# Kernel optimization log

Hardware: AMD Instinct MI355X
Metric: run time of the kernel (lower is better)

The kernel has to match this reference:

```python
import jax, jax.numpy as jnp
import numpy as np

IN_CH, OUT_CH, H, E, DOUT, MODES = 512, 512, 8, 64, 64, 64
B, LQ, LKV = 32, 1024, 1024


def setup_inputs() -> dict:
    key = jax.random.key(0)
    kq, kk, kv, kwr, kwi = jax.random.split(key, 5)
    scale = 1.0 / (IN_CH * OUT_CH)
    return {
        "q": jax.random.normal(kq, (B, LQ, H, E), jnp.float32),
        "k": jax.random.normal(kk, (B, LKV, H, E), jnp.float32),
        "v": jax.random.normal(kv, (B, LKV, H, E), jnp.float32),
        "mask": jnp.zeros((B, LQ), jnp.bool_),
        # complex parameter stored as (real, imag) pair; torch init is scale*rand -> U[0, scale)
        "weights_real": scale * jax.random.uniform(kwr, (H, E, DOUT, MODES), jnp.float32),
        "weights_imag": scale * jax.random.uniform(kwi, (H, E, DOUT, MODES), jnp.float32),
        # 'lowest' mode selection: arange(modes); all modes valid since LQ//2+1 > 63
        "index_q": jnp.arange(MODES, dtype=jnp.int32),
        "index_kv": jnp.arange(MODES, dtype=jnp.int32),
    }


def reference(q, k, v, mask, weights_real, weights_imag, index_q, index_kv):
    Lq = q.shape[1]
    # (B, L, H, E) -> (B, H, E, L)
    xq = jnp.transpose(q, (0, 2, 3, 1))
    xk = jnp.transpose(k, (0, 2, 3, 1))
    xq_ft = jnp.fft.rfft(xq.astype(jnp.float32), axis=-1)   # (B,H,E,Lq//2+1) c64
    xk_ft = jnp.fft.rfft(xk.astype(jnp.float32), axis=-1)
    xq_sel = xq_ft[..., index_q]    # (B,H,E,Mq) mode gather
    xk_sel = xk_ft[..., index_kv]   # (B,H,E,Mkv)
    # complex attention scores: xq_sel.mT @ xk_sel (no conjugation, matching torch)
    xqk = jnp.einsum("bhex,bhey->bhxy", xq_sel, xk_sel)     # (B,H,Mq,Mkv)
    # 'tanh' activation applied to real and imag parts separately
    xqk = jax.lax.complex(jnp.tanh(xqk.real), jnp.tanh(xqk.imag))
    w = jax.lax.complex(weights_real, weights_imag)         # (H,E,DOUT,Mq)
    xqkvw = jnp.einsum("bhxy,bhey,heox->bhox", xqk, xk_sel, w)  # (B,H,DOUT,Mq)
    # scatter selected modes back into zero spectrum, then inverse FFT
    freq_len_q = Lq // 2 + 1
    out_ft = jnp.zeros(xqkvw.shape[:3] + (freq_len_q,), jnp.complex64)
    out_ft = out_ft.at[..., index_q].set(xqkvw)
    out = jnp.fft.irfft(out_ft / (IN_CH * OUT_CH), n=Lq, axis=-1)  # (B,H,DOUT,Lq)
    return out.astype(q.dtype)
```

## Files before the change

kernel.cpp:

```cpp
#include <hip/hip_runtime.h>
#include <math.h>

#define OFF_WTR   262144u
#define OFF_WTI   2359296u
#define OFF_XQR   4456448u
#define OFF_XQI   5505024u
#define OFF_XKR   6553600u
#define OFF_XKI   7602176u
#define OFF_UR    8650752u
#define OFF_UI    9699328u
#define OFF_YR    10747904u
#define OFF_YI    11796480u

#define PI_F 3.14159265358979323846f

typedef __attribute__((ext_vector_type(8))) short bf16x8;
typedef __attribute__((ext_vector_type(4))) float f32x4;

__device__ inline unsigned short f2bf(float f) {
    unsigned u = __float_as_uint(f);
    unsigned r = u + 0x7FFFu + ((u >> 16) & 1u);
    return (unsigned short)(r >> 16);
}
__device__ inline float bf2f(unsigned short h) {
    return __uint_as_float(((unsigned)h) << 16);
}
__device__ inline void make_hilo8(const float* s, bf16x8& h, bf16x8& l) {
#pragma unroll
    for (int j = 0; j < 8; ++j) {
        unsigned short hb = f2bf(s[j]);
        h[j] = (short)hb;
        l[j] = (short)f2bf(s[j] - bf2f(hb));
    }
}
__device__ inline float twval(int m, int t, bool neg_sin) {
    int r = (m * t) & 1023;
    float ang = (float)r * (2.0f * PI_F / 1024.0f);
    float s, c;
    sincosf(ang, &s, &c);
    return neg_sin ? -s : c;
}

__global__ void k_tables(unsigned short* __restrict__ tab) {
    int idx = blockIdx.x * 256 + threadIdx.x;
    {
        int j = idx & 7, lane = (idx >> 3) & 63, nt = (idx >> 9) & 7, kt = idx >> 12;
        int k = kt * 32 + ((lane >> 4) << 3) + j;
        int n = nt * 16 + (lane & 15);
        float v = twval(n & 63, k, n >= 64);
        unsigned short hb = f2bf(v);
        tab[idx] = hb;
        tab[131072 + idx] = f2bf(v - bf2f(hb));
    }
    {
        int j = idx & 7, lane = (idx >> 3) & 63, ks = (idx >> 9) & 3, nt = idx >> 11;
        int kap = ks * 32 + ((lane >> 4) << 3) + j;
        int t = nt * 16 + (lane & 15);
        float v = twval(kap & 63, t, kap >= 64);
        unsigned short hb = f2bf(v);
        tab[262144 + idx] = hb;
        tab[393216 + idx] = f2bf(v - bf2f(hb));
    }
}

__global__ __launch_bounds__(256) void k_wt(const float* __restrict__ wr,
                                            const float* __restrict__ wi,
                                            float* __restrict__ ws) {
    __shared__ float tile[64 * 65];
    int he = blockIdx.x;
    int h = he >> 6, e = he & 63;
    const float* srcs[2] = { wr + (size_t)he * 4096, wi + (size_t)he * 4096 };
    float* dsts[2] = { ws + OFF_WTR, ws + OFF_WTI };
    for (int p = 0; p < 2; ++p) {
        __syncthreads();
        {
            int x = threadIdx.x & 63, orow = threadIdx.x >> 6;
            for (int i = 0; i < 16; ++i) {
                int o = orow * 16 + i;
                tile[o * 65 + x] = srcs[p][o * 64 + x];
            }
        }
        __syncthreads();
        {
            int o = threadIdx.x & 63, xrow = threadIdx.x >> 6;
            for (int i = 0; i < 16; ++i) {
                int x = xrow * 16 + i;
                dsts[p][(((size_t)h * 64 + x) * 64 + e) * 64 + o] = tile[o * 65 + x];
            }
        }
    }
}

__global__ __launch_bounds__(256, 2) void k_dft(const float* __restrict__ q,
                                                const float* __restrict__ kk,
                                                float* __restrict__ ws) {
    int blk = blockIdx.x;
    int src = blk >> 8;
    int bh = blk & 255;
    int b = bh >> 3, h = bh & 7;
    const float* A = src ? kk : q;
    const unsigned short* BDH = (const unsigned short*)ws;
    const unsigned short* BDL = BDH + 131072;

    __shared__ float Ald[64 * 68];

    int tid = threadIdx.x;
    int lane = tid & 63, wv = tid >> 6;
    int mhalf = wv & 1, nhalf = wv >> 1;

    f32x4 acc[2][4];
#pragma unroll
    for (int a = 0; a < 2; ++a)
#pragma unroll
        for (int c = 0; c < 4; ++c) acc[a][c] = (f32x4){0.f, 0.f, 0.f, 0.f};

    for (int kc = 0; kc < 16; ++kc) {
        __syncthreads();
        int t0 = kc * 64;
        int e0 = (tid & 15) * 4;
#pragma unroll
        for (int it = 0; it < 4; ++it) {
            int tl = it * 16 + (tid >> 4);
            float4 a = *(const float4*)(A + (((size_t)b * 1024 + t0 + tl) * 8 + h) * 64 + e0);
            Ald[(e0 + 0) * 68 + tl] = a.x;
            Ald[(e0 + 1) * 68 + tl] = a.y;
            Ald[(e0 + 2) * 68 + tl] = a.z;
            Ald[(e0 + 3) * 68 + tl] = a.w;
        }
        __syncthreads();
#pragma unroll
        for (int k2 = 0; k2 < 2; ++k2) {
            int ktile = kc * 2 + k2;
            bf16x8 ah[2], al[2];
#pragma unroll
            for (int mt = 0; mt < 2; ++mt) {
                int e = mhalf * 32 + mt * 16 + (lane & 15);
                int tt = k2 * 32 + (lane >> 4) * 8;
                float4 p0 = *(const float4*)&Ald[e * 68 + tt];
                float4 p1 = *(const float4*)&Ald[e * 68 + tt + 4];
                float f[8] = { p0.x, p0.y, p0.z, p0.w, p1.x, p1.y, p1.z, p1.w };
                make_hilo8(f, ah[mt], al[mt]);
            }
#pragma unroll
            for (int ntl = 0; ntl < 4; ++ntl) {
                int nt = nhalf * 4 + ntl;
                size_t off = (((size_t)ktile * 8 + nt) * 64 + lane) * 8;
                bf16x8 bh = *(const bf16x8*)(BDH + off);
                bf16x8 bl = *(const bf16x8*)(BDL + off);
#pragma unroll
                for (int mt = 0; mt < 2; ++mt) {
                    acc[mt][ntl] = __builtin_amdgcn_mfma_f32_16x16x32_bf16(ah[mt], bh, acc[mt][ntl], 0, 0, 0);
                    acc[mt][ntl] = __builtin_amdgcn_mfma_f32_16x16x32_bf16(ah[mt], bl, acc[mt][ntl], 0, 0, 0);
                    acc[mt][ntl] = __builtin_amdgcn_mfma_f32_16x16x32_bf16(al[mt], bh, acc[mt][ntl], 0, 0, 0);
                }
            }
        }
    }

    float* outR = ws + (src ? OFF_XKR : OFF_XQR) + (size_t)bh * 4096;
    float* outI = ws + (src ? OFF_XKI : OFF_XQI) + (size_t)bh * 4096;
#pragma unroll
    for (int mt = 0; mt < 2; ++mt)
#pragma unroll
        for (int ntl = 0; ntl < 4; ++ntl) {
            int n = (nhalf * 4 + ntl) * 16 + (lane & 15);
            float* dst = (n < 64) ? (outR + (n & 63)) : (outI + (n & 63));
            int erow0 = mhalf * 32 + mt * 16 + (lane >> 4) * 4;
#pragma unroll
            for (int r = 0; r < 4; ++r)
                dst[(erow0 + r) * 64] = acc[mt][ntl][r];
        }
}

__global__ __launch_bounds__(256, 1) void k_attn(float* __restrict__ ws) {
    __shared__ float bufA[8192];
    __shared__ float bufB[8192];
    int bh = blockIdx.x;
    int tid = threadIdx.x;
    const float* XqR = ws + OFF_XQR + (size_t)bh * 4096;
    const float* XqI = ws + OFF_XQI + (size_t)bh * 4096;
    const float* XkR = ws + OFF_XKR + (size_t)bh * 4096;
    const float* XkI = ws + OFF_XKI + (size_t)bh * 4096;
    for (int i = tid; i < 4096; i += 256) {
        bufA[i] = XqR[i]; bufA[4096 + i] = XqI[i];
        bufB[i] = XkR[i]; bufB[4096 + i] = XkI[i];
    }
    __syncthreads();

    int x4 = tid & 15, y4 = tid >> 4;
    int x0 = x4 * 4, y0 = y4 * 4;
    float Sr[4][4], Si[4][4];
#pragma unroll
    for (int a = 0; a < 4; ++a)
#pragma unroll
        for (int bidx = 0; bidx < 4; ++bidx) { Sr[a][bidx] = 0.f; Si[a][bidx] = 0.f; }
#pragma unroll 8
    for (int e = 0; e < 64; ++e) {
        float4 qr = *(const float4*)&bufA[e * 64 + x0];
        float4 qi = *(const float4*)&bufA[4096 + e * 64 + x0];
        float4 kr = *(const float4*)&bufB[e * 64 + y0];
        float4 ki = *(const float4*)&bufB[4096 + e * 64 + y0];
        float qra[4] = { qr.x, qr.y, qr.z, qr.w };
        float qia[4] = { qi.x, qi.y, qi.z, qi.w };
        float kra[4] = { kr.x, kr.y, kr.z, kr.w };
        float kia[4] = { ki.x, ki.y, ki.z, ki.w };
#pragma unroll
        for (int xi = 0; xi < 4; ++xi)
#pragma unroll
            for (int yi = 0; yi < 4; ++yi) {
                Sr[xi][yi] += qra[xi] * kra[yi] - qia[xi] * kia[yi];
                Si[xi][yi] += qra[xi] * kia[yi] + qia[xi] * kra[yi];
            }
    }
#pragma unroll
    for (int xi = 0; xi < 4; ++xi)
#pragma unroll
        for (int yi = 0; yi < 4; ++yi) {
            Sr[xi][yi] = tanhf(Sr[xi][yi]);
            Si[xi][yi] = tanhf(Si[xi][yi]);
        }
    __syncthreads();

#pragma unroll
    for (int xi = 0; xi < 4; ++xi)
#pragma unroll
        for (int yi = 0; yi < 4; ++yi) {
            bufA[(y0 + yi) * 64 + x0 + xi] = Sr[xi][yi];
            bufA[4096 + (y0 + yi) * 64 + x0 + xi] = Si[xi][yi];
        }
    float tR[16], tI[16];
#pragma unroll
    for (int j = 0; j < 16; ++j) {
        int idx = tid + 256 * j;
        tR[j] = bufB[idx]; tI[j] = bufB[4096 + idx];
    }
    __syncthreads();
#pragma unroll
    for (int j = 0; j < 16; ++j) {
        int idx = tid + 256 * j;
        int e = idx >> 6, m = idx & 63;
        bufB[m * 64 + e] = tR[j];
        bufB[4096 + m * 64 + e] = tI[j];
    }
    __syncthreads();

    int e4 = tid & 15, xb4 = tid >> 4;
    int e0 = e4 * 4, xb0 = xb4 * 4;
    float uR[4][4], uI[4][4];
#pragma unroll
    for (int a = 0; a < 4; ++a)
#pragma unroll
        for (int bidx = 0; bidx < 4; ++bidx) { uR[a][bidx] = 0.f; uI[a][bidx] = 0.f; }
#pragma unroll 8
    for (int y = 0; y < 64; ++y) {
        float4 sr = *(const float4*)&bufA[y * 64 + xb0];
        float4 si = *(const float4*)&bufA[4096 + y * 64 + xb0];
        float4 kr = *(const float4*)&bufB[y * 64 + e0];
        float4 ki = *(const float4*)&bufB[4096 + y * 64 + e0];
        float sra[4] = { sr.x, sr.y, sr.z, sr.w };
        float sia[4] = { si.x, si.y, si.z, si.w };
        float kra[4] = { kr.x, kr.y, kr.z, kr.w };
        float kia[4] = { ki.x, ki.y, ki.z, ki.w };
#pragma unroll
        for (int ei = 0; ei < 4; ++ei)
#pragma unroll
            for (int xi = 0; xi < 4; ++xi) {
                uR[ei][xi] += sra[xi] * kra[ei] - sia[xi] * kia[ei];
                uI[ei][xi] += sra[xi] * kia[ei] + sia[xi] * kra[ei];
            }
    }
    int b = bh >> 3, h = bh & 7;
    float* uRp = ws + OFF_UR;
    float* uIp = ws + OFF_UI;
#pragma unroll
    for (int xi = 0; xi < 4; ++xi) {
        size_t base = (((size_t)h * 64 + (xb0 + xi)) * 32 + b) * 64 + e0;
        float4 vr = { uR[0][xi], uR[1][xi], uR[2][xi], uR[3][xi] };
        float4 vi = { uI[0][xi], uI[1][xi], uI[2][xi], uI[3][xi] };
        *(float4*)&uRp[base] = vr;
        *(float4*)&uIp[base] = vi;
    }
}

__global__ __launch_bounds__(256, 2) void k_uw(float* __restrict__ ws) {
    __shared__ float su[2 * 2176];
    __shared__ float sw[2 * 4096];
    int hx = blockIdx.x;
    int tid = threadIdx.x;
    const float* uRp = ws + OFF_UR + (size_t)hx * 2048;
    const float* uIp = ws + OFF_UI + (size_t)hx * 2048;
    const float* wRp = ws + OFF_WTR + (size_t)hx * 4096;
    const float* wIp = ws + OFF_WTI + (size_t)hx * 4096;
    for (int i = tid; i < 2048; i += 256) {
        int b = i >> 6, e = i & 63;
        su[b * 68 + e] = uRp[i];
        su[2176 + b * 68 + e] = uIp[i];
    }
    for (int i = tid; i < 4096; i += 256) {
        sw[i] = wRp[i];
        sw[4096 + i] = wIp[i];
    }
    __syncthreads();
    int o16 = tid & 15, b8 = tid >> 4;
    int o0 = o16 * 4, b0 = b8 * 2;
    float aR[2][4], aI[2][4];
#pragma unroll
    for (int bi = 0; bi < 2; ++bi)
#pragma unroll
        for (int oi = 0; oi < 4; ++oi) { aR[bi][oi] = 0.f; aI[bi][oi] = 0.f; }
#pragma unroll 8
    for (int e = 0; e < 64; ++e) {
        float u0r = su[(b0 + 0) * 68 + e], u0i = su[2176 + (b0 + 0) * 68 + e];
        float u1r = su[(b0 + 1) * 68 + e], u1i = su[2176 + (b0 + 1) * 68 + e];
        float4 wr = *(const float4*)&sw[e * 64 + o0];
        float4 wi = *(const float4*)&sw[4096 + e * 64 + o0];
        float wra[4] = { wr.x, wr.y, wr.z, wr.w };
        float wia[4] = { wi.x, wi.y, wi.z, wi.w };
#pragma unroll
        for (int oi = 0; oi < 4; ++oi) {
            aR[0][oi] += u0r * wra[oi] - u0i * wia[oi];
            aI[0][oi] += u0r * wia[oi] + u0i * wra[oi];
            aR[1][oi] += u1r * wra[oi] - u1i * wia[oi];
            aI[1][oi] += u1r * wia[oi] + u1i * wra[oi];
        }
    }
    float* YRp = ws + OFF_YR + (size_t)hx * 2048;
    float* YIp = ws + OFF_YI + (size_t)hx * 2048;
#pragma unroll
    for (int bi = 0; bi < 2; ++bi) {
        float4 vr = { aR[bi][0], aR[bi][1], aR[bi][2], aR[bi][3] };
        float4 vi = { aI[bi][0], aI[bi][1], aI[bi][2], aI[bi][3] };
        *(float4*)&YRp[(b0 + bi) * 64 + o0] = vr;
        *(float4*)&YIp[(b0 + bi) * 64 + o0] = vi;
    }
}

__global__ __launch_bounds__(512, 2) void k_idft(const float* __restrict__ ws,
                                                 float* __restrict__ out) {
    __shared__ float Acoef[64 * 132];
    int bh = blockIdx.x;
    int b = bh >> 3, h = bh & 7;
    int tid = threadIdx.x;
    int lane = tid & 63, wv = tid >> 6;
    const float S0 = 3.7252902984619140625e-09f;
    const float* YRp = ws + OFF_YR;
    const float* YIp = ws + OFF_YI;
    const unsigned short* BIH = (const unsigned short*)ws + 262144;
    const unsigned short* BIL = (const unsigned short*)ws + 393216;

    for (int i = tid; i < 4096; i += 512) {
        int m = i >> 6, o = i & 63;
        size_t src = ((size_t)h * 64 + m) * 2048 + (size_t)b * 64 + o;
        float sca = (m == 0 ? 1.f : 2.f) * S0;
        Acoef[o * 132 + m] = YRp[src] * sca;
        Acoef[o * 132 + 64 + m] = YIp[src] * sca;
    }
    __syncthreads();

    bf16x8 ah[4][4], al[4][4];
#pragma unroll
    for (int mt = 0; mt < 4; ++mt)
#pragma unroll
        for (int ks = 0; ks < 4; ++ks) {
            int o = mt * 16 + (lane & 15);
            int kap0 = ks * 32 + (lane >> 4) * 8;
            float4 p0 = *(const float4*)&Acoef[o * 132 + kap0];
            float4 p1 = *(const float4*)&Acoef[o * 132 + kap0 + 4];
            float f[8] = { p0.x, p0.y, p0.z, p0.w, p1.x, p1.y, p1.z, p1.w };
            make_hilo8(f, ah[mt][ks], al[mt][ks]);
        }

    float* outp = out + ((size_t)b * 8 + h) * 65536;
#pragma unroll 2
    for (int ntl = 0; ntl < 8; ++ntl) {
        int nt = wv * 8 + ntl;
        f32x4 acc[4];
#pragma unroll
        for (int mt = 0; mt < 4; ++mt) acc[mt] = (f32x4){0.f, 0.f, 0.f, 0.f};
#pragma unroll
        for (int ks = 0; ks < 4; ++ks) {
            size_t off = (((size_t)nt * 4 + ks) * 64 + lane) * 8;
            bf16x8 bh = *(const bf16x8*)(BIH + off);
            bf16x8 bl = *(const bf16x8*)(BIL + off);
#pragma unroll
            for (int mt = 0; mt < 4; ++mt) {
                acc[mt] = __builtin_amdgcn_mfma_f32_16x16x32_bf16(ah[mt][ks], bh, acc[mt], 0, 0, 0);
                acc[mt] = __builtin_amdgcn_mfma_f32_16x16x32_bf16(ah[mt][ks], bl, acc[mt], 0, 0, 0);
                acc[mt] = __builtin_amdgcn_mfma_f32_16x16x32_bf16(al[mt][ks], bh, acc[mt], 0, 0, 0);
            }
        }
        int t = nt * 16 + (lane & 15);
#pragma unroll
        for (int mt = 0; mt < 4; ++mt) {
            int o0 = mt * 16 + (lane >> 4) * 4;
#pragma unroll
            for (int r = 0; r < 4; ++r)
                outp[(size_t)(o0 + r) * 1024 + t] = acc[mt][r];
        }
    }
}

extern "C" void kernel_launch(void* const* d_in, const int* in_sizes, int n_in,
                              void* d_out, int out_size, void* d_ws, size_t ws_size,
                              hipStream_t stream) {
    const float* q = (const float*)d_in[0];
    const float* k = (const float*)d_in[1];
    const float* wr = (const float*)d_in[4];
    const float* wi = (const float*)d_in[5];
    float* out = (float*)d_out;
    float* ws = (float*)d_ws;

    k_tables<<<512, 256, 0, stream>>>((unsigned short*)d_ws);
    k_wt<<<512, 256, 0, stream>>>(wr, wi, ws);
    k_dft<<<512, 256, 0, stream>>>(q, k, ws);
    k_attn<<<256, 256, 0, stream>>>(ws);
    k_uw<<<512, 256, 0, stream>>>(ws);
    k_idft<<<256, 512, 0, stream>>>(ws, out);
}
```

Measured before the change: 341.1 us.

## Move attention and weight contractions to split-bf16 MFMA and split DFT/IDFT work

The scalar FP32 complex matmuls in k_attn and k_uw are replaced with 3-pass hi/lo bf16 MFMA products. The imaginary-part negation is done by flipping the sign bit of the bf16 operands. k_dft now uses 512 threads that split the time dimension in two and combine the partial sums through shared memory, and it reads inputs straight from global memory instead of staging a transposed LDS tile. k_idft launches twice as many blocks, each handling half of the output time tiles, to raise parallelism. The hi/lo split may change accuracy slightly, and the uncoalesced strided global loads in the DFT could cost bandwidth.

```diff
diff --git a/kernel.cpp b/kernel.cpp
--- a/kernel.cpp
+++ b/kernel.cpp
@@ -33,6 +33,12 @@
         l[j] = (short)f2bf(s[j] - bf2f(hb));
     }
 }
+__device__ inline bf16x8 neg8(bf16x8 v) {
+    bf16x8 r;
+#pragma unroll
+    for (int j = 0; j < 8; ++j) r[j] = (short)(((unsigned short)v[j]) ^ 0x8000u);
+    return r;
+}
 __device__ inline float twval(int m, int t, bool neg_sin) {
     int r = (m * t) & 1023;
     float ang = (float)r * (2.0f * PI_F / 1024.0f);
@@ -40,6 +46,11 @@
     sincosf(ang, &s, &c);
     return neg_sin ? -s : c;
 }
+
+#define MFMA3(AH, AL, BH, BL, ACC)                                          \
+    ACC = __builtin_amdgcn_mfma_f32_16x16x32_bf16(AH, BH, ACC, 0, 0, 0);    \
+    ACC = __builtin_amdgcn_mfma_f32_16x16x32_bf16(AH, BL, ACC, 0, 0, 0);    \
+    ACC = __builtin_amdgcn_mfma_f32_16x16x32_bf16(AL, BH, ACC, 0, 0, 0);
 
 __global__ void k_tables(unsigned short* __restrict__ tab) {
     int idx = blockIdx.x * 256 + threadIdx.x;
@@ -91,22 +102,20 @@
     }
 }
 
-__global__ __launch_bounds__(256, 2) void k_dft(const float* __restrict__ q,
+__global__ __launch_bounds__(512, 4) void k_dft(const float* __restrict__ q,
                                                 const float* __restrict__ kk,
                                                 float* __restrict__ ws) {
     int blk = blockIdx.x;
     int src = blk >> 8;
-    int bh = blk & 255;
-    int b = bh >> 3, h = bh & 7;
+    int bhi = blk & 255;
+    int b = bhi >> 3, h = bhi & 7;
     const float* A = src ? kk : q;
     const unsigned short* BDH = (const unsigned short*)ws;
     const unsigned short* BDL = BDH + 131072;
 
-    __shared__ float Ald[64 * 68];
-
     int tid = threadIdx.x;
     int lane = tid & 63, wv = tid >> 6;
-    int mhalf = wv & 1, nhalf = wv >> 1;
+    int kh = wv & 1, mh = (wv >> 1) & 1, nh = wv >> 2;
 
     f32x4 acc[2][4];
 #pragma unroll
@@ -114,232 +123,277 @@
 #pragma unroll
         for (int c = 0; c < 4; ++c) acc[a][c] = (f32x4){0.f, 0.f, 0.f, 0.f};
 
-    for (int kc = 0; kc < 16; ++kc) {
-        __syncthreads();
-        int t0 = kc * 64;
-        int e0 = (tid & 15) * 4;
-#pragma unroll
-        for (int it = 0; it < 4; ++it) {
-            int tl = it * 16 + (tid >> 4);
-            float4 a = *(const float4*)(A + (((size_t)b * 1024 + t0 + tl) * 8 + h) * 64 + e0);
-            Ald[(e0 + 0) * 68 + tl] = a.x;
-            Ald[(e0 + 1) * 68 + tl] = a.y;
-            Ald[(e0 + 2) * 68 + tl] = a.z;
-            Ald[(e0 + 3) * 68 + tl] = a.w;
-        }
-        __syncthreads();
+    for (int kc = 0; kc < 8; ++kc) {
+        int tbase = kh * 512 + kc * 64;
+        bf16x8 ah[2][2], al[2][2];
+#pragma unroll
+        for (int mt = 0; mt < 2; ++mt) {
+            int e = mh * 32 + mt * 16 + (lane & 15);
+#pragma unroll
+            for (int k2 = 0; k2 < 2; ++k2) {
+                int t0 = tbase + k2 * 32 + (lane >> 4) * 8;
+                float f[8];
+#pragma unroll
+                for (int j = 0; j < 8; ++j)
+                    f[j] = A[(((size_t)b * 1024 + t0 + j) * 8 + h) * 64 + e];
+                make_hilo8(f, ah[mt][k2], al[mt][k2]);
+            }
+        }
 #pragma unroll
         for (int k2 = 0; k2 < 2; ++k2) {
-            int ktile = kc * 2 + k2;
-            bf16x8 ah[2], al[2];
-#pragma unroll
-            for (int mt = 0; mt < 2; ++mt) {
-                int e = mhalf * 32 + mt * 16 + (lane & 15);
-                int tt = k2 * 32 + (lane >> 4) * 8;
-                float4 p0 = *(const float4*)&Ald[e * 68 + tt];
-                float4 p1 = *(const float4*)&Ald[e * 68 + tt + 4];
-                float f[8] = { p0.x, p0.y, p0.z, p0.w, p1.x, p1.y, p1.z, p1.w };
-                make_hilo8(f, ah[mt], al[mt]);
-            }
+            int ktile = kh * 16 + kc * 2 + k2;
 #pragma unroll
             for (int ntl = 0; ntl < 4; ++ntl) {
-                int nt = nhalf * 4 + ntl;
+                int nt = nh * 4 + ntl;
                 size_t off = (((size_t)ktile * 8 + nt) * 64 + lane) * 8;
-                bf16x8 bh = *(const bf16x8*)(BDH + off);
-                bf16x8 bl = *(const bf16x8*)(BDL + off);
+                bf16x8 tbh = *(const bf16x8*)(BDH + off);
+                bf16x8 tbl = *(const bf16x8*)(BDL + off);
 #pragma unroll
                 for (int mt = 0; mt < 2; ++mt) {
-                    acc[mt][ntl] = __builtin_amdgcn_mfma_f32_16x16x32_bf16(ah[mt], bh, acc[mt][ntl], 0, 0, 0);
-                    acc[mt][ntl] = __builtin_amdgcn_mfma_f32_16x16x32_bf16(ah[mt], bl, acc[mt][ntl], 0, 0, 0);
-                    acc[mt][ntl] = __builtin_amdgcn_mfma_f32_16x16x32_bf16(al[mt], bh, acc[mt][ntl], 0, 0, 0);
+                    MFMA3(ah[mt][k2], al[mt][k2], tbh, tbl, acc[mt][ntl]);
                 }
             }
         }
     }
 
-    float* outR = ws + (src ? OFF_XKR : OFF_XQR) + (size_t)bh * 4096;
-    float* outI = ws + (src ? OFF_XKI : OFF_XQI) + (size_t)bh * 4096;
-#pragma unroll
-    for (int mt = 0; mt < 2; ++mt)
-#pragma unroll
-        for (int ntl = 0; ntl < 4; ++ntl) {
-            int n = (nhalf * 4 + ntl) * 16 + (lane & 15);
-            float* dst = (n < 64) ? (outR + (n & 63)) : (outI + (n & 63));
-            int erow0 = mhalf * 32 + mt * 16 + (lane >> 4) * 4;
-#pragma unroll
-            for (int r = 0; r < 4; ++r)
-                dst[(erow0 + r) * 64] = acc[mt][ntl][r];
-        }
+    __shared__ float red[8192];
+    int pair = wv >> 1;
+    if (kh == 1) {
+#pragma unroll
+        for (int mt = 0; mt < 2; ++mt)
+#pragma unroll
+            for (int ntl = 0; ntl < 4; ++ntl)
+#pragma unroll
+                for (int r = 0; r < 4; ++r)
+                    red[pair * 2048 + ((mt * 4 + ntl) * 4 + r) * 64 + lane] = acc[mt][ntl][r];
+    }
+    __syncthreads();
+    if (kh == 0) {
+        float* outR = ws + (src ? OFF_XKR : OFF_XQR) + (size_t)bhi * 4096;
+        float* outI = ws + (src ? OFF_XKI : OFF_XQI) + (size_t)bhi * 4096;
+#pragma unroll
+        for (int mt = 0; mt < 2; ++mt)
+#pragma unroll
+            for (int ntl = 0; ntl < 4; ++ntl) {
+#pragma unroll
+                for (int r = 0; r < 4; ++r)
+                    acc[mt][ntl][r] += red[pair * 2048 + ((mt * 4 + ntl) * 4 + r) * 64 + lane];
+                int n = (nh * 4 + ntl) * 16 + (lane & 15);
+                float* dst = (n < 64) ? (outR + n) : (outI + (n - 64));
+                int erow0 = mh * 32 + mt * 16 + (lane >> 4) * 4;
+#pragma unroll
+                for (int r = 0; r < 4; ++r)
+                    dst[(erow0 + r) * 64] = acc[mt][ntl][r];
+            }
+    }
 }
 
 __global__ __launch_bounds__(256, 1) void k_attn(float* __restrict__ ws) {
-    __shared__ float bufA[8192];
-    __shared__ float bufB[8192];
-    int bh = blockIdx.x;
-    int tid = threadIdx.x;
-    const float* XqR = ws + OFF_XQR + (size_t)bh * 4096;
-    const float* XqI = ws + OFF_XQI + (size_t)bh * 4096;
-    const float* XkR = ws + OFF_XKR + (size_t)bh * 4096;
-    const float* XkI = ws + OFF_XKI + (size_t)bh * 4096;
+    __shared__ float sKR[64 * 65], sKI[64 * 65];
+    __shared__ float sQR[64 * 65], sQI[64 * 65];
+    int bhi = blockIdx.x;
+    int b = bhi >> 3, h = bhi & 7;
+    int tid = threadIdx.x, lane = tid & 63, wv = tid >> 6;
+    const float* XqR = ws + OFF_XQR + (size_t)bhi * 4096;
+    const float* XqI = ws + OFF_XQI + (size_t)bhi * 4096;
+    const float* XkR = ws + OFF_XKR + (size_t)bhi * 4096;
+    const float* XkI = ws + OFF_XKI + (size_t)bhi * 4096;
     for (int i = tid; i < 4096; i += 256) {
-        bufA[i] = XqR[i]; bufA[4096 + i] = XqI[i];
-        bufB[i] = XkR[i]; bufB[4096 + i] = XkI[i];
+        int e = i >> 6, m = i & 63;
+        sQR[e * 65 + m] = XqR[i];
+        sQI[e * 65 + m] = XqI[i];
+        sKR[e * 65 + m] = XkR[i];
+        sKI[e * 65 + m] = XkI[i];
     }
     __syncthreads();
 
-    int x4 = tid & 15, y4 = tid >> 4;
-    int x0 = x4 * 4, y0 = y4 * 4;
-    float Sr[4][4], Si[4][4];
-#pragma unroll
-    for (int a = 0; a < 4; ++a)
-#pragma unroll
-        for (int bidx = 0; bidx < 4; ++bidx) { Sr[a][bidx] = 0.f; Si[a][bidx] = 0.f; }
-#pragma unroll 8
-    for (int e = 0; e < 64; ++e) {
-        float4 qr = *(const float4*)&bufA[e * 64 + x0];
-        float4 qi = *(const float4*)&bufA[4096 + e * 64 + x0];
-        float4 kr = *(const float4*)&bufB[e * 64 + y0];
-        float4 ki = *(const float4*)&bufB[4096 + e * 64 + y0];
-        float qra[4] = { qr.x, qr.y, qr.z, qr.w };
-        float qia[4] = { qi.x, qi.y, qi.z, qi.w };
-        float kra[4] = { kr.x, kr.y, kr.z, kr.w };
-        float kia[4] = { ki.x, ki.y, ki.z, ki.w };
-#pragma unroll
-        for (int xi = 0; xi < 4; ++xi)
-#pragma unroll
-            for (int yi = 0; yi < 4; ++yi) {
-                Sr[xi][yi] += qra[xi] * kra[yi] - qia[xi] * kia[yi];
-                Si[xi][yi] += qra[xi] * kia[yi] + qia[xi] * kra[yi];
-            }
-    }
-#pragma unroll
-    for (int xi = 0; xi < 4; ++xi)
-#pragma unroll
-        for (int yi = 0; yi < 4; ++yi) {
-            Sr[xi][yi] = tanhf(Sr[xi][yi]);
-            Si[xi][yi] = tanhf(Si[xi][yi]);
-        }
+    int x = wv * 16 + (lane & 15);
+    bf16x8 aRh[2], aRl[2], aIh[2], aIl[2], aInh[2], aInl[2];
+#pragma unroll
+    for (int k2 = 0; k2 < 2; ++k2) {
+        float fr[8], fi[8];
+#pragma unroll
+        for (int j = 0; j < 8; ++j) {
+            int e = k2 * 32 + (lane >> 4) * 8 + j;
+            fr[j] = sQR[e * 65 + x];
+            fi[j] = sQI[e * 65 + x];
+        }
+        make_hilo8(fr, aRh[k2], aRl[k2]);
+        make_hilo8(fi, aIh[k2], aIl[k2]);
+        aInh[k2] = neg8(aIh[k2]);
+        aInl[k2] = neg8(aIl[k2]);
+    }
     __syncthreads();
 
-#pragma unroll
-    for (int xi = 0; xi < 4; ++xi)
-#pragma unroll
-        for (int yi = 0; yi < 4; ++yi) {
-            bufA[(y0 + yi) * 64 + x0 + xi] = Sr[xi][yi];
-            bufA[4096 + (y0 + yi) * 64 + x0 + xi] = Si[xi][yi];
-        }
-    float tR[16], tI[16];
-#pragma unroll
-    for (int j = 0; j < 16; ++j) {
-        int idx = tid + 256 * j;
-        tR[j] = bufB[idx]; tI[j] = bufB[4096 + idx];
+    f32x4 Sr[4], Si[4];
+#pragma unroll
+    for (int c = 0; c < 4; ++c) { Sr[c] = (f32x4){0.f,0.f,0.f,0.f}; Si[c] = (f32x4){0.f,0.f,0.f,0.f}; }
+#pragma unroll
+    for (int k2 = 0; k2 < 2; ++k2) {
+#pragma unroll
+        for (int nt = 0; nt < 4; ++nt) {
+            float gr[8], gi[8];
+            int y = nt * 16 + (lane & 15);
+#pragma unroll
+            for (int j = 0; j < 8; ++j) {
+                int e = k2 * 32 + (lane >> 4) * 8 + j;
+                gr[j] = sKR[e * 65 + y];
+                gi[j] = sKI[e * 65 + y];
+            }
+            bf16x8 bRh, bRl, bIh, bIl;
+            make_hilo8(gr, bRh, bRl);
+            make_hilo8(gi, bIh, bIl);
+            MFMA3(aRh[k2], aRl[k2], bRh, bRl, Sr[nt]);
+            MFMA3(aInh[k2], aInl[k2], bIh, bIl, Sr[nt]);
+            MFMA3(aRh[k2], aRl[k2], bIh, bIl, Si[nt]);
+            MFMA3(aIh[k2], aIl[k2], bRh, bRl, Si[nt]);
+        }
+    }
+#pragma unroll
+    for (int nt = 0; nt < 4; ++nt)
+#pragma unroll
+        for (int r = 0; r < 4; ++r) {
+            Sr[nt][r] = tanhf(Sr[nt][r]);
+            Si[nt][r] = tanhf(Si[nt][r]);
+        }
+#pragma unroll
+    for (int nt = 0; nt < 4; ++nt) {
+        int y = nt * 16 + (lane & 15);
+        int xr0 = wv * 16 + (lane >> 4) * 4;
+#pragma unroll
+        for (int r = 0; r < 4; ++r) {
+            sQR[(xr0 + r) * 65 + y] = Sr[nt][r];
+            sQI[(xr0 + r) * 65 + y] = Si[nt][r];
+        }
     }
     __syncthreads();
-#pragma unroll
-    for (int j = 0; j < 16; ++j) {
-        int idx = tid + 256 * j;
-        int e = idx >> 6, m = idx & 63;
-        bufB[m * 64 + e] = tR[j];
-        bufB[4096 + m * 64 + e] = tI[j];
-    }
-    __syncthreads();
-
-    int e4 = tid & 15, xb4 = tid >> 4;
-    int e0 = e4 * 4, xb0 = xb4 * 4;
-    float uR[4][4], uI[4][4];
-#pragma unroll
-    for (int a = 0; a < 4; ++a)
-#pragma unroll
-        for (int bidx = 0; bidx < 4; ++bidx) { uR[a][bidx] = 0.f; uI[a][bidx] = 0.f; }
-#pragma unroll 8
-    for (int y = 0; y < 64; ++y) {
-        float4 sr = *(const float4*)&bufA[y * 64 + xb0];
-        float4 si = *(const float4*)&bufA[4096 + y * 64 + xb0];
-        float4 kr = *(const float4*)&bufB[y * 64 + e0];
-        float4 ki = *(const float4*)&bufB[4096 + y * 64 + e0];
-        float sra[4] = { sr.x, sr.y, sr.z, sr.w };
-        float sia[4] = { si.x, si.y, si.z, si.w };
-        float kra[4] = { kr.x, kr.y, kr.z, kr.w };
-        float kia[4] = { ki.x, ki.y, ki.z, ki.w };
-#pragma unroll
-        for (int ei = 0; ei < 4; ++ei)
-#pragma unroll
-            for (int xi = 0; xi < 4; ++xi) {
-                uR[ei][xi] += sra[xi] * kra[ei] - sia[xi] * kia[ei];
-                uI[ei][xi] += sra[xi] * kia[ei] + sia[xi] * kra[ei];
-            }
-    }
-    int b = bh >> 3, h = bh & 7;
+
+    bf16x8 cRh[2], cRl[2], cIh[2], cIl[2], cInh[2], cInl[2];
+#pragma unroll
+    for (int k2 = 0; k2 < 2; ++k2) {
+        float fr[8], fi[8];
+#pragma unroll
+        for (int j = 0; j < 8; ++j) {
+            int y = k2 * 32 + (lane >> 4) * 8 + j;
+            fr[j] = sQR[x * 65 + y];
+            fi[j] = sQI[x * 65 + y];
+        }
+        make_hilo8(fr, cRh[k2], cRl[k2]);
+        make_hilo8(fi, cIh[k2], cIl[k2]);
+        cInh[k2] = neg8(cIh[k2]);
+        cInl[k2] = neg8(cIl[k2]);
+    }
+
+    f32x4 Ur[4], Ui[4];
+#pragma unroll
+    for (int c = 0; c < 4; ++c) { Ur[c] = (f32x4){0.f,0.f,0.f,0.f}; Ui[c] = (f32x4){0.f,0.f,0.f,0.f}; }
+#pragma unroll
+    for (int k2 = 0; k2 < 2; ++k2) {
+#pragma unroll
+        for (int nt = 0; nt < 4; ++nt) {
+            float gr[8], gi[8];
+            int e = nt * 16 + (lane & 15);
+#pragma unroll
+            for (int j = 0; j < 8; ++j) {
+                int y = k2 * 32 + (lane >> 4) * 8 + j;
+                gr[j] = sKR[e * 65 + y];
+                gi[j] = sKI[e * 65 + y];
+            }
+            bf16x8 bRh, bRl, bIh, bIl;
+            make_hilo8(gr, bRh, bRl);
+            make_hilo8(gi, bIh, bIl);
+            MFMA3(cRh[k2], cRl[k2], bRh, bRl, Ur[nt]);
+            MFMA3(cInh[k2], cInl[k2], bIh, bIl, Ur[nt]);
+            MFMA3(cRh[k2], cRl[k2], bIh, bIl, Ui[nt]);
+            MFMA3(cIh[k2], cIl[k2], bRh, bRl, Ui[nt]);
+        }
+    }
     float* uRp = ws + OFF_UR;
     float* uIp = ws + OFF_UI;
 #pragma unroll
-    for (int xi = 0; xi < 4; ++xi) {
-        size_t base = (((size_t)h * 64 + (xb0 + xi)) * 32 + b) * 64 + e0;
-        float4 vr = { uR[0][xi], uR[1][xi], uR[2][xi], uR[3][xi] };
-        float4 vi = { uI[0][xi], uI[1][xi], uI[2][xi], uI[3][xi] };
-        *(float4*)&uRp[base] = vr;
-        *(float4*)&uIp[base] = vi;
+    for (int nt = 0; nt < 4; ++nt) {
+        int e = nt * 16 + (lane & 15);
+        int xr0 = wv * 16 + (lane >> 4) * 4;
+#pragma unroll
+        for (int r = 0; r < 4; ++r) {
+            size_t base = (((size_t)h * 64 + xr0 + r) * 32 + b) * 64 + e;
+            uRp[base] = Ur[nt][r];
+            uIp[base] = Ui[nt][r];
+        }
     }
 }
 
 __global__ __launch_bounds__(256, 2) void k_uw(float* __restrict__ ws) {
-    __shared__ float su[2 * 2176];
-    __shared__ float sw[2 * 4096];
     int hx = blockIdx.x;
-    int tid = threadIdx.x;
+    int tid = threadIdx.x, lane = tid & 63, wv = tid >> 6;
     const float* uRp = ws + OFF_UR + (size_t)hx * 2048;
     const float* uIp = ws + OFF_UI + (size_t)hx * 2048;
     const float* wRp = ws + OFF_WTR + (size_t)hx * 4096;
     const float* wIp = ws + OFF_WTI + (size_t)hx * 4096;
-    for (int i = tid; i < 2048; i += 256) {
-        int b = i >> 6, e = i & 63;
-        su[b * 68 + e] = uRp[i];
-        su[2176 + b * 68 + e] = uIp[i];
-    }
-    for (int i = tid; i < 4096; i += 256) {
-        sw[i] = wRp[i];
-        sw[4096 + i] = wIp[i];
-    }
-    __syncthreads();
-    int o16 = tid & 15, b8 = tid >> 4;
-    int o0 = o16 * 4, b0 = b8 * 2;
-    float aR[2][4], aI[2][4];
-#pragma unroll
-    for (int bi = 0; bi < 2; ++bi)
-#pragma unroll
-        for (int oi = 0; oi < 4; ++oi) { aR[bi][oi] = 0.f; aI[bi][oi] = 0.f; }
-#pragma unroll 8
-    for (int e = 0; e < 64; ++e) {
-        float u0r = su[(b0 + 0) * 68 + e], u0i = su[2176 + (b0 + 0) * 68 + e];
-        float u1r = su[(b0 + 1) * 68 + e], u1i = su[2176 + (b0 + 1) * 68 + e];
-        float4 wr = *(const float4*)&sw[e * 64 + o0];
-        float4 wi = *(const float4*)&sw[4096 + e * 64 + o0];
-        float wra[4] = { wr.x, wr.y, wr.z, wr.w };
-        float wia[4] = { wi.x, wi.y, wi.z, wi.w };
-#pragma unroll
-        for (int oi = 0; oi < 4; ++oi) {
-            aR[0][oi] += u0r * wra[oi] - u0i * wia[oi];
-            aI[0][oi] += u0r * wia[oi] + u0i * wra[oi];
-            aR[1][oi] += u1r * wra[oi] - u1i * wia[oi];
-            aI[1][oi] += u1r * wia[oi] + u1i * wra[oi];
+
+    bf16x8 aRh[2][2], aRl[2][2], aIh[2][2], aIl[2][2], aInh[2][2], aInl[2][2];
+#pragma unroll
+    for (int mt = 0; mt < 2; ++mt) {
+        int bb = mt * 16 + (lane & 15);
+#pragma unroll
+        for (int k2 = 0; k2 < 2; ++k2) {
+            int e0 = k2 * 32 + (lane >> 4) * 8;
+            float fr[8], fi[8];
+#pragma unroll
+            for (int j = 0; j < 8; ++j) {
+                fr[j] = uRp[bb * 64 + e0 + j];
+                fi[j] = uIp[bb * 64 + e0 + j];
+            }
+            make_hilo8(fr, aRh[mt][k2], aRl[mt][k2]);
+            make_hilo8(fi, aIh[mt][k2], aIl[mt][k2]);
+            aInh[mt][k2] = neg8(aIh[mt][k2]);
+            aInl[mt][k2] = neg8(aIl[mt][k2]);
+        }
+    }
+
+    f32x4 Yr[2], Yi[2];
+#pragma unroll
+    for (int mt = 0; mt < 2; ++mt) { Yr[mt] = (f32x4){0.f,0.f,0.f,0.f}; Yi[mt] = (f32x4){0.f,0.f,0.f,0.f}; }
+    int o = wv * 16 + (lane & 15);
+#pragma unroll
+    for (int k2 = 0; k2 < 2; ++k2) {
+        float gr[8], gi[8];
+#pragma unroll
+        for (int j = 0; j < 8; ++j) {
+            int e = k2 * 32 + (lane >> 4) * 8 + j;
+            gr[j] = wRp[e * 64 + o];
+            gi[j] = wIp[e * 64 + o];
+        }
+        bf16x8 bRh, bRl, bIh, bIl;
+        make_hilo8(gr, bRh, bRl);
+        make_hilo8(gi, bIh, bIl);
+#pragma unroll
+        for (int mt = 0; mt < 2; ++mt) {
+            MFMA3(aRh[mt][k2], aRl[mt][k2], bRh, bRl, Yr[mt]);
+            MFMA3(aInh[mt][k2], aInl[mt][k2], bIh, bIl, Yr[mt]);
+            MFMA3(aRh[mt][k2], aRl[mt][k2], bIh, bIl, Yi[mt]);
+            MFMA3(aIh[mt][k2], aIl[mt][k2], bRh, bRl, Yi[mt]);
         }
     }
     float* YRp = ws + OFF_YR + (size_t)hx * 2048;
     float* YIp = ws + OFF_YI + (size_t)hx * 2048;
 #pragma unroll
-    for (int bi = 0; bi < 2; ++bi) {
-        float4 vr = { aR[bi][0], aR[bi][1], aR[bi][2], aR[bi][3] };
-        float4 vi = { aI[bi][0], aI[bi][1], aI[bi][2], aI[bi][3] };
-        *(float4*)&YRp[(b0 + bi) * 64 + o0] = vr;
-        *(float4*)&YIp[(b0 + bi) * 64 + o0] = vi;
+    for (int mt = 0; mt < 2; ++mt) {
+#pragma unroll
+        for (int r = 0; r < 4; ++r) {
+            int bb = mt * 16 + (lane >> 4) * 4 + r;
+            YRp[bb * 64 + o] = Yr[mt][r];
+            YIp[bb * 64 + o] = Yi[mt][r];
+        }
     }
 }
 
 __global__ __launch_bounds__(512, 2) void k_idft(const float* __restrict__ ws,
                                                  float* __restrict__ out) {
     __shared__ float Acoef[64 * 132];
-    int bh = blockIdx.x;
-    int b = bh >> 3, h = bh & 7;
+    int blk = blockIdx.x;
+    int bhi = blk >> 1, nhf = blk & 1;
+    int b = bhi >> 3, h = bhi & 7;
     int tid = threadIdx.x;
     int lane = tid & 63, wv = tid >> 6;
     const float S0 = 3.7252902984619140625e-09f;
@@ -372,21 +426,19 @@
 
     float* outp = out + ((size_t)b * 8 + h) * 65536;
 #pragma unroll 2
-    for (int ntl = 0; ntl < 8; ++ntl) {
-        int nt = wv * 8 + ntl;
+    for (int ntl = 0; ntl < 4; ++ntl) {
+        int nt = nhf * 32 + wv * 4 + ntl;
         f32x4 acc[4];
 #pragma unroll
         for (int mt = 0; mt < 4; ++mt) acc[mt] = (f32x4){0.f, 0.f, 0.f, 0.f};
 #pragma unroll
         for (int ks = 0; ks < 4; ++ks) {
             size_t off = (((size_t)nt * 4 + ks) * 64 + lane) * 8;
-            bf16x8 bh = *(const bf16x8*)(BIH + off);
-            bf16x8 bl = *(const bf16x8*)(BIL + off);
+            bf16x8 tbh = *(const bf16x8*)(BIH + off);
+            bf16x8 tbl = *(const bf16x8*)(BIL + off);
 #pragma unroll
             for (int mt = 0; mt < 4; ++mt) {
-                acc[mt] = __builtin_amdgcn_mfma_f32_16x16x32_bf16(ah[mt][ks], bh, acc[mt], 0, 0, 0);
-                acc[mt] = __builtin_amdgcn_mfma_f32_16x16x32_bf16(ah[mt][ks], bl, acc[mt], 0, 0, 0);
-                acc[mt] = __builtin_amdgcn_mfma_f32_16x16x32_bf16(al[mt][ks], bh, acc[mt], 0, 0, 0);
+                MFMA3(ah[mt][ks], al[mt][ks], tbh, tbl, acc[mt]);
             }
         }
         int t = nt * 16 + (lane & 15);
@@ -412,8 +464,8 @@
 
     k_tables<<<512, 256, 0, stream>>>((unsigned short*)d_ws);
     k_wt<<<512, 256, 0, stream>>>(wr, wi, ws);
-    k_dft<<<512, 256, 0, stream>>>(q, k, ws);
+    k_dft<<<512, 512, 0, stream>>>(q, k, ws);
     k_attn<<<256, 256, 0, stream>>>(ws);
     k_uw<<<512, 256, 0, stream>>>(ws);
-    k_idft<<<256, 512, 0, stream>>>(ws, out);
-}
+    k_idft<<<512, 512, 0, stream>>>(ws, out);
+}
```

After: 309.5 us. 1.1x faster.
